# Optimization experiments

Measured on AMD Instinct MI355X. Metric: run time of the kernel, lower is better.

## Reference

```python
import jax, jax.numpy as jnp
import numpy as np

FEATURE_DIM = 128
NUM_EDGES = 640000
NUM_NODES = 40000


def setup_inputs() -> dict:
    key = jax.random.key(0)
    ks = jax.random.split(key, 10)
    d = FEATURE_DIM
    scale = 1.0 / np.sqrt(d)
    inp = {
        "messages": jax.random.normal(ks[0], (NUM_EDGES, d), dtype=jnp.float32),
        "receivers": jax.random.randint(ks[1], (NUM_EDGES,), 0, NUM_NODES, dtype=jnp.int32),
        "num_segments": NUM_NODES,
        "Wk": jax.random.normal(ks[2], (d, d), dtype=jnp.float32) * scale,
        "bk": jnp.zeros((d,), dtype=jnp.float32),
        "Wv": jax.random.normal(ks[3], (d, d), dtype=jnp.float32) * scale,
        "bv": jnp.zeros((d,), dtype=jnp.float32),
        "Wq": jax.random.normal(ks[4], (d, d), dtype=jnp.float32) * scale,
        "bq": jnp.zeros((d,), dtype=jnp.float32),
        "Wo": jax.random.normal(ks[5], (d, d), dtype=jnp.float32) * scale,
        "bo": jnp.zeros((d,), dtype=jnp.float32),
    }
    return inp


def reference(messages, receivers, num_segments, Wk, bk, Wv, bv, Wq, bq, Wo, bo):
    d = messages.shape[-1]
    # per-edge key/value projections
    keys = messages @ Wk + bk            # [E, d]
    values = messages @ Wv + bv          # [E, d]
    # node-level summed messages -> queries
    summed = jax.ops.segment_sum(messages, receivers, num_segments)  # [N, d]
    queries = summed @ Wq + bq                                       # [N, d]
    # scalar attention score per edge (dot over full feature dim)
    msg_q = queries[receivers]                                       # [E, d]
    scores = jnp.sum(msg_q * keys, axis=-1) / jnp.sqrt(jnp.float32(d))  # [E]
    # segment softmax over edges sharing a receiver
    max_s = jax.ops.segment_max(scores, receivers, num_segments)     # [N]
    exp_s = jnp.exp(scores - max_s[receivers])                       # [E]
    sum_e = jax.ops.segment_sum(exp_s, receivers, num_segments)      # [N]
    attn = exp_s / (sum_e[receivers] + 1e-08)                        # [E]
    # weighted scatter-sum of values, then output projection
    agg = jax.ops.segment_sum(values * attn[:, None], receivers, num_segments)  # [N, d]
    return agg @ Wo + bo
```

## Files before the change

### kernel.cpp

```cpp
#include <hip/hip_runtime.h>

#define D 128
#define RSQRT_D 0.088388347648318440550f
#define NEG_HUGE -3.4e38f
#define NPB 8
#define CAP 288
#define DTHR 20.0f

#define FMA4(acc, s, b) { acc.x += (s)*(b).x; acc.y += (s)*(b).y; acc.z += (s)*(b).z; acc.w += (s)*(b).w; }
#define ADD4(acc, b) { acc.x += (b).x; acc.y += (b).y; acc.z += (b).z; acc.w += (b).w; }
#define MRG4(a) { a.x += __shfl_xor(a.x,32); a.y += __shfl_xor(a.y,32); a.z += __shfl_xor(a.z,32); a.w += __shfl_xor(a.w,32); }
#define SCL4(a, f) { a.x *= (f); a.y *= (f); a.z *= (f); a.w *= (f); }
#define Z4 make_float4(0.f,0.f,0.f,0.f)

#define MERGE_HALVES(mi, si, ci) { \
    float mo_ = __shfl_xor(mi, 32); \
    float so_ = __shfl_xor(si, 32); \
    float4 co_; co_.x = __shfl_xor(ci.x, 32); co_.y = __shfl_xor(ci.y, 32); \
    co_.z = __shfl_xor(ci.z, 32); co_.w = __shfl_xor(ci.w, 32); \
    float mt_ = fmaxf(mi, mo_); \
    float e0_ = __expf(mi - mt_), e1_ = __expf(mo_ - mt_); \
    si = si * e0_ + so_ * e1_; \
    ci.x = ci.x * e0_ + co_.x * e1_; ci.y = ci.y * e0_ + co_.y * e1_; \
    ci.z = ci.z * e0_ + co_.z * e1_; ci.w = ci.w * e0_ + co_.w * e1_; \
}

__global__ __launch_bounds__(256) void prep_kernel(
    const float* __restrict__ Wq, const float* __restrict__ Wk,
    const float* __restrict__ bq, const float* __restrict__ bk,
    const float* __restrict__ Wv, const float* __restrict__ Wo,
    const float* __restrict__ bv,
    float* __restrict__ Wqk, float* __restrict__ bqk,
    float* __restrict__ wqb, float* __restrict__ bqb,
    float* __restrict__ Wvo, float* __restrict__ bvo,
    int* __restrict__ zbase, int zcount) {
    int bid = blockIdx.x, t = threadIdx.x;
    if (bid < 64) {
        int i = bid * 2 + (t >> 7), j = t & 127;
        float a1 = 0.f, a2 = 0.f;
        for (int u = 0; u < D; ++u) {
            a1 += Wq[i * D + u] * Wk[j * D + u];
            a2 += Wv[i * D + u] * Wo[u * D + j];
        }
        Wqk[i * D + j] = a1;
        Wvo[i * D + j] = a2;
    } else if (bid == 64) {
        if (t < D) {
            int j = t;
            float a1 = 0.f, a2 = 0.f, a3 = 0.f;
            for (int u = 0; u < D; ++u) {
                a1 += bq[u] * Wk[j * D + u];
                a2 += Wq[j * D + u] * bk[u];
                a3 += bv[u] * Wo[u * D + j];
            }
            bqk[j] = a1; wqb[j] = a2; bvo[j] = a3;
            if (j == 0) {
                float b = 0.f;
                for (int u = 0; u < D; ++u) b += bq[u] * bk[u];
                *bqb = b;
            }
        }
    } else {
        int idx = (bid - 65) * 256 + t;
        if (idx < zcount) zbase[idx] = 0;
    }
}

__global__ void hist_kernel(const int* __restrict__ recv, int* __restrict__ cnt, int E) {
    int i = blockIdx.x * blockDim.x + threadIdx.x;
    int base = i << 2;
    if (base + 3 < E) {
        int4 r = *(const int4*)(recv + base);
        atomicAdd(&cnt[r.x], 1);
        atomicAdd(&cnt[r.y], 1);
        atomicAdd(&cnt[r.z], 1);
        atomicAdd(&cnt[r.w], 1);
    } else {
        for (int u = base; u < E; ++u) atomicAdd(&cnt[recv[u]], 1);
    }
}

__global__ __launch_bounds__(1024) void scan_kernel(const int* __restrict__ cnt,
                                                    int* __restrict__ start, int N) {
    __shared__ int wsum[16];
    __shared__ int chunk_total;
    int t = threadIdx.x;
    int w = t >> 6, lane = t & 63;
    int running = 0;
    const int4* cnt4 = (const int4*)cnt;
    int nIter = (N + 4095) >> 12;
    int4 v = make_int4(0, 0, 0, 0);
    {
        int i = t << 2;
        if (i < N) v = cnt4[i >> 2];
    }
    for (int it = 0; it < nIter; ++it) {
        int4 vn = make_int4(0, 0, 0, 0);
        {
            int i = ((it + 1) << 12) + (t << 2);
            if (it + 1 < nIter && i < N) vn = cnt4[i >> 2];
        }
        int s0 = v.x, s1 = s0 + v.y, s2 = s1 + v.z, s3 = s2 + v.w;
        int x = s3;
#pragma unroll
        for (int off = 1; off < 64; off <<= 1) {
            int y = __shfl_up(x, off);
            if (lane >= off) x += y;
        }
        if (lane == 63) wsum[w] = x;
        __syncthreads();
        if (w == 0 && lane < 16) {
            int s = wsum[lane];
#pragma unroll
            for (int off = 1; off < 16; off <<= 1) {
                int y = __shfl_up(s, off);
                if (lane >= off) s += y;
            }
            wsum[lane] = s;
            if (lane == 15) chunk_total = s;
        }
        __syncthreads();
        int waveoff = (w == 0) ? 0 : wsum[w - 1];
        int tb = running + waveoff + (x - s3);
        int i = (it << 12) + (t << 2);
        if (i < N) ((int4*)start)[i >> 2] = make_int4(tb, tb + s0, tb + s1, tb + s2);
        running += chunk_total;
        __syncthreads();
        v = vn;
    }
    if (t == 0) start[N] = running;
}

__global__ void fill_kernel(const int* __restrict__ recv, const int* __restrict__ start,
                            int* __restrict__ cursor, int* __restrict__ eidx, int E) {
    int e = blockIdx.x * blockDim.x + threadIdx.x;
    if (e >= E) return;
    int r = recv[e];
    int p = atomicAdd(&cursor[r], 1);
    eidx[start[r] + p] = e;
}

__device__ __forceinline__ float hdot32(float4 f, float4 q) {
    float p = f.x * q.x + f.y * q.y + f.z * q.z + f.w * q.w;
    p += __shfl_xor(p, 1); p += __shfl_xor(p, 2); p += __shfl_xor(p, 4);
    p += __shfl_xor(p, 8); p += __shfl_xor(p, 16);
    return p;
}

#define P1STEP(u, Fx) { \
    int r = j + h + 2 * (u); \
    float4 g_ = Fx; \
    float mk_ = (r < b4) ? 1.f : 0.f; \
    g_.x *= mk_; g_.y *= mk_; g_.z *= mk_; g_.w *= mk_; \
    if (r < b1)      { ADD4(a0, g_); } \
    else if (r < b2) { ADD4(a1, g_); } \
    else if (r < b3) { ADD4(a2, g_); } \
    else             { ADD4(a3, g_); } \
}

#define P3STEP(u, Fx) { \
    int r = j + h + 2 * (u); \
    bool valid_ = r < b4; \
    float4 f_ = Fx; \
    float4 qv_ = (r < b1) ? q0 : (r < b2) ? q1 : (r < b3) ? q2 : q3; \
    float qbv_ = (r < b1) ? qb0 : (r < b2) ? qb1 : (r < b3) ? qb2 : qb3; \
    float sc_ = (hdot32(f_, qv_) + qbv_) * RSQRT_D; \
    float msel_ = (r < b1) ? m0 : (r < b2) ? m1 : (r < b3) ? m2 : m3; \
    if (valid_ && sc_ > msel_ + DTHR) { \
        float fac_ = __expf(msel_ - sc_); \
        if (r < b1)      { sm0 *= fac_; SCL4(c0, fac_); m0 = sc_; } \
        else if (r < b2) { sm1 *= fac_; SCL4(c1, fac_); m1 = sc_; } \
        else if (r < b3) { sm2 *= fac_; SCL4(c2, fac_); m2 = sc_; } \
        else             { sm3 *= fac_; SCL4(c3, fac_); m3 = sc_; } \
        msel_ = sc_; \
    } \
    float wgt_ = valid_ ? __expf(sc_ - msel_) : 0.f; \
    if (r < b1)      { sm0 += wgt_; FMA4(c0, wgt_, f_); } \
    else if (r < b2) { sm1 += wgt_; FMA4(c1, wgt_, f_); } \
    else if (r < b3) { sm2 += wgt_; FMA4(c2, wgt_, f_); } \
    else             { sm3 += wgt_; FMA4(c3, wgt_, f_); } \
}

#define P1G(jo, Ra, Rb, Rc, Rd) { int j = b0 + (jo); P1STEP(0, Ra); P1STEP(1, Rb); P1STEP(2, Rc); P1STEP(3, Rd); }
#define P3G(jo, Ra, Rb, Rc, Rd) { int j = b0 + (jo); P3STEP(0, Ra); P3STEP(1, Rb); P3STEP(2, Rc); P3STEP(3, Rd); }

__global__ __launch_bounds__(128, 3) void mega_kernel(
    const float* __restrict__ msg, const int* __restrict__ eidx,
    const int* __restrict__ start,
    const float* __restrict__ Wqk, const float* __restrict__ bqk,
    const float* __restrict__ wqb, const float* __restrict__ bqbp,
    const float* __restrict__ Wvo, const float* __restrict__ bvo,
    const float* __restrict__ bo,
    float* __restrict__ out, int N) {
    __shared__ float4 sums4[NPB * 32];
    __shared__ float4 qks4[NPB * 32];
    __shared__ int eidx_s[CAP];
    __shared__ float sat[NPB];

    int t = threadIdx.x;
    int lane = t & 63, w = t >> 6;
    int h = lane >> 5;
    int k = lane & 31;
    int base = blockIdx.x * NPB;
    const float4* msg4 = (const float4*)msg;

    int nendB = min(base + NPB, N);
    int s0B = start[base];
    int cntB = start[nendB] - s0B;
    int cc = min(cntB, CAP);
    for (int i = t; i < cc; i += 128) eidx_s[i] = eidx[s0B + i];

    int n0 = base + w * 4;
    int b0 = start[min(n0 + 0, N)] - s0B;
    int b1 = start[min(n0 + 1, N)] - s0B;
    int b2 = start[min(n0 + 2, N)] - s0B;
    int b3 = start[min(n0 + 3, N)] - s0B;
    int b4 = start[min(n0 + 4, N)] - s0B;

    __syncthreads();

    auto loadrow = [&](int r) -> float4 {
        int rI = min(r, b4 - 1);
        int e = (rI < CAP) ? eidx_s[rI] : eidx[s0B + rI];
        return msg4[(size_t)e * 32 + k];
    };

    float4 R00 = Z4, R01 = Z4, R02 = Z4, R03 = Z4,
           R10 = Z4, R11 = Z4, R12 = Z4, R13 = Z4,
           R20 = Z4, R21 = Z4, R22 = Z4, R23 = Z4,
           R30 = Z4, R31 = Z4, R32 = Z4, R33 = Z4,
           R40 = Z4, R41 = Z4, R42 = Z4, R43 = Z4,
           R50 = Z4, R51 = Z4, R52 = Z4, R53 = Z4;

    float4 a0 = Z4, a1 = Z4, a2 = Z4, a3 = Z4;
    if (b0 < b4) {
        R00 = loadrow(b0 + h +  0); R01 = loadrow(b0 + h +  2); R02 = loadrow(b0 + h +  4); R03 = loadrow(b0 + h +  6);
        R10 = loadrow(b0 + h +  8); R11 = loadrow(b0 + h + 10); R12 = loadrow(b0 + h + 12); R13 = loadrow(b0 + h + 14);
        R20 = loadrow(b0 + h + 16); R21 = loadrow(b0 + h + 18); R22 = loadrow(b0 + h + 20); R23 = loadrow(b0 + h + 22);
        R30 = loadrow(b0 + h + 24); R31 = loadrow(b0 + h + 26); R32 = loadrow(b0 + h + 28); R33 = loadrow(b0 + h + 30);
        R40 = loadrow(b0 + h + 32); R41 = loadrow(b0 + h + 34); R42 = loadrow(b0 + h + 36); R43 = loadrow(b0 + h + 38);
        R50 = loadrow(b0 + h + 40); R51 = loadrow(b0 + h + 42); R52 = loadrow(b0 + h + 44); R53 = loadrow(b0 + h + 46);
        P1G( 0, R00, R01, R02, R03);
        P1G( 8, R10, R11, R12, R13);
        P1G(16, R20, R21, R22, R23);
        P1G(24, R30, R31, R32, R33);
        P1G(32, R40, R41, R42, R43);
        P1G(40, R50, R51, R52, R53);
        int j = b0 + 48;
        if (j < b4) {
            float4 F0 = loadrow(j + h), F1 = loadrow(j + h + 2);
            for (;;) {
                int jn = j + 4;
                bool more = jn < b4;
                float4 G0, G1;
                if (more) { G0 = loadrow(jn + h); G1 = loadrow(jn + h + 2); }
                P1STEP(0, F0); P1STEP(1, F1);
                if (!more) break;
                F0 = G0; F1 = G1; j = jn;
            }
        }
    }
    MRG4(a0); MRG4(a1); MRG4(a2); MRG4(a3);
    if (lane < 32) {
        sums4[(w * 4 + 0) * 32 + k] = a0;
        sums4[(w * 4 + 1) * 32 + k] = a1;
        sums4[(w * 4 + 2) * 32 + k] = a2;
        sums4[(w * 4 + 3) * 32 + k] = a3;
    }
    __syncthreads();

    {
        int c = t & 31, slot = t >> 5;
        const float4* B4 = (const float4*)Wqk;
        float4 acc0 = ((const float4*)bqk)[c];
        float4 acc1 = acc0;
        for (int i = 0; i < D; i += 4) {
            float4 aA = sums4[slot * 32 + (i >> 2)];
            float4 aB = sums4[(slot + 4) * 32 + (i >> 2)];
            float4 w0 = B4[(i + 0) * 32 + c];
            float4 w1 = B4[(i + 1) * 32 + c];
            float4 w2 = B4[(i + 2) * 32 + c];
            float4 w3 = B4[(i + 3) * 32 + c];
            FMA4(acc0, aA.x, w0); FMA4(acc0, aA.y, w1); FMA4(acc0, aA.z, w2); FMA4(acc0, aA.w, w3);
            FMA4(acc1, aB.x, w0); FMA4(acc1, aB.y, w1); FMA4(acc1, aB.z, w2); FMA4(acc1, aB.w, w3);
        }
        qks4[slot * 32 + c] = acc0;
        qks4[(slot + 4) * 32 + c] = acc1;
    }
    __syncthreads();

    {
        float4 wv = ((const float4*)wqb)[k];
        float bqb = bqbp[0];
        float4 sv0 = sums4[(w * 4 + 0) * 32 + k];
        float4 sv1 = sums4[(w * 4 + 1) * 32 + k];
        float4 sv2 = sums4[(w * 4 + 2) * 32 + k];
        float4 sv3 = sums4[(w * 4 + 3) * 32 + k];
        float qb0 = hdot32(sv0, wv) + bqb;
        float qb1 = hdot32(sv1, wv) + bqb;
        float qb2 = hdot32(sv2, wv) + bqb;
        float qb3 = hdot32(sv3, wv) + bqb;
        float4 q0 = qks4[(w * 4 + 0) * 32 + k];
        float4 q1 = qks4[(w * 4 + 1) * 32 + k];
        float4 q2 = qks4[(w * 4 + 2) * 32 + k];
        float4 q3 = qks4[(w * 4 + 3) * 32 + k];

        float m0 = NEG_HUGE, m1 = NEG_HUGE, m2 = NEG_HUGE, m3 = NEG_HUGE;
        float sm0 = 0.f, sm1 = 0.f, sm2 = 0.f, sm3 = 0.f;
        float4 c0 = Z4, c1 = Z4, c2 = Z4, c3 = Z4;
        if (b0 < b4) {
            P3G( 0, R00, R01, R02, R03);
            P3G( 8, R10, R11, R12, R13);
            P3G(16, R20, R21, R22, R23);
            P3G(24, R30, R31, R32, R33);
            P3G(32, R40, R41, R42, R43);
            P3G(40, R50, R51, R52, R53);
            int j = b0 + 48;
            if (j < b4) {
                float4 F0 = loadrow(j + h), F1 = loadrow(j + h + 2);
                for (;;) {
                    int jn = j + 4;
                    bool more = jn < b4;
                    float4 G0, G1;
                    if (more) { G0 = loadrow(jn + h); G1 = loadrow(jn + h + 2); }
                    P3STEP(0, F0); P3STEP(1, F1);
                    if (!more) break;
                    F0 = G0; F1 = G1; j = jn;
                }
            }
        }
        MERGE_HALVES(m0, sm0, c0);
        MERGE_HALVES(m1, sm1, c1);
        MERGE_HALVES(m2, sm2, c2);
        MERGE_HALVES(m3, sm3, c3);
        float inv0 = 1.f / (sm0 + 1e-8f);
        float inv1 = 1.f / (sm1 + 1e-8f);
        float inv2 = 1.f / (sm2 + 1e-8f);
        float inv3 = 1.f / (sm3 + 1e-8f);
        if (lane < 32) {
            sums4[(w * 4 + 0) * 32 + k] = make_float4(c0.x * inv0, c0.y * inv0, c0.z * inv0, c0.w * inv0);
            sums4[(w * 4 + 1) * 32 + k] = make_float4(c1.x * inv1, c1.y * inv1, c1.z * inv1, c1.w * inv1);
            sums4[(w * 4 + 2) * 32 + k] = make_float4(c2.x * inv2, c2.y * inv2, c2.z * inv2, c2.w * inv2);
            sums4[(w * 4 + 3) * 32 + k] = make_float4(c3.x * inv3, c3.y * inv3, c3.z * inv3, c3.w * inv3);
        }
        if (lane == 0) {
            sat[w * 4 + 0] = sm0 * inv0;
            sat[w * 4 + 1] = sm1 * inv1;
            sat[w * 4 + 2] = sm2 * inv2;
            sat[w * 4 + 3] = sm3 * inv3;
        }
    }
    __syncthreads();

    {
        int c = t & 31, slot = t >> 5;
        const float4* B4 = (const float4*)Wvo;
        float4 bo4 = ((const float4*)bo)[c];
        float4 bv4 = ((const float4*)bvo)[c];
        float sa0 = sat[slot], sa1 = sat[slot + 4];
        float4 acc0 = make_float4(bo4.x + sa0 * bv4.x, bo4.y + sa0 * bv4.y,
                                  bo4.z + sa0 * bv4.z, bo4.w + sa0 * bv4.w);
        float4 acc1 = make_float4(bo4.x + sa1 * bv4.x, bo4.y + sa1 * bv4.y,
                                  bo4.z + sa1 * bv4.z, bo4.w + sa1 * bv4.w);
        for (int i = 0; i < D; i += 4) {
            float4 aA = sums4[slot * 32 + (i >> 2)];
            float4 aB = sums4[(slot + 4) * 32 + (i >> 2)];
            float4 d0 = B4[(i + 0) * 32 + c];
            float4 d1 = B4[(i + 1) * 32 + c];
            float4 d2 = B4[(i + 2) * 32 + c];
            float4 d3 = B4[(i + 3) * 32 + c];
            FMA4(acc0, aA.x, d0); FMA4(acc0, aA.y, d1); FMA4(acc0, aA.z, d2); FMA4(acc0, aA.w, d3);
            FMA4(acc1, aB.x, d0); FMA4(acc1, aB.y, d1); FMA4(acc1, aB.z, d2); FMA4(acc1, aB.w, d3);
        }
        int nA = base + slot, nB = base + slot + 4;
        if (nA < N) ((float4*)(out + (size_t)nA * D))[c] = acc0;
        if (nB < N) ((float4*)(out + (size_t)nB * D))[c] = acc1;
    }
}


extern "C" void kernel_launch(void* const* d_in, const int* in_sizes, int n_in,
                              void* d_out, int out_size, void* d_ws, size_t ws_size,
                              hipStream_t stream) {
    const float* msg = (const float*)d_in[0];
    const int* recv = (const int*)d_in[1];
    const float* Wk = (const float*)d_in[3];
    const float* bk = (const float*)d_in[4];
    const float* Wv = (const float*)d_in[5];
    const float* bv = (const float*)d_in[6];
    const float* Wq = (const float*)d_in[7];
    const float* bq = (const float*)d_in[8];
    const float* Wo = (const float*)d_in[9];
    const float* bo = (const float*)d_in[10];
    float* out = (float*)d_out;

    int E = in_sizes[0] / D;
    int N = out_size / D;

    char* wsb = (char*)d_ws;
    size_t o = 0;
    auto alloc = [&](size_t elems) {
        void* p = wsb + o;
        o += (elems * 4 + 63) & ~(size_t)63;
        return p;
    };

    int* cnt    = (int*)alloc(2 * (size_t)N);
    int* cursor = cnt + N;
    int* start  = (int*)alloc(N + 1);
    int* eidx   = (int*)alloc(E);
    float* Wqk  = (float*)alloc(D * D);
    float* bqk  = (float*)alloc(D);
    float* wqb  = (float*)alloc(D);
    float* bqb  = (float*)alloc(1);
    float* Wvo  = (float*)alloc(D * D);
    float* bvo  = (float*)alloc(D);

    int zcount = 2 * N;
    int zblocks = (zcount + 255) / 256;
    prep_kernel<<<65 + zblocks, 256, 0, stream>>>(Wq, Wk, bq, bk, Wv, Wo, bv,
                                                  Wqk, bqk, wqb, bqb, Wvo, bvo,
                                                  cnt, zcount);
    int E4 = (E + 3) / 4;
    int nbE4 = (E4 + 255) / 256;
    hist_kernel<<<nbE4, 256, 0, stream>>>(recv, cnt, E);
    scan_kernel<<<1, 1024, 0, stream>>>(cnt, start, N);
    int nbE = (E + 255) / 256;
    fill_kernel<<<nbE, 256, 0, stream>>>(recv, start, cursor, eidx, E);
    mega_kernel<<<(N + NPB - 1) / NPB, 128, 0, stream>>>(msg, eidx, start, Wqk, bqk, wqb, bqb,
                                                         Wvo, bvo, bo, out, N);
}
```

Measured before the change: 680.7 us.

## Stream edge rows through an async global-to-LDS ring instead of register caching

Drops the 24 float4 rows each lane kept in registers between the summation pass and the softmax pass. Both passes now stream edge rows through an 8-deep per-wave LDS ring, filled with global_load_lds and throttled by explicit vmcnt waits. The lower register pressure lets the launch bound rise from 3 to 4 blocks per CU. In exchange, the second pass re-reads message rows from memory, relying on L2 hits. There is also a possible race where a ring slot is reused right after it is read, with no explicit LDS wait.

```diff
diff --git a/kernel.cpp b/kernel.cpp
--- a/kernel.cpp
+++ b/kernel.cpp
@@ -12,6 +12,14 @@
 #define MRG4(a) { a.x += __shfl_xor(a.x,32); a.y += __shfl_xor(a.y,32); a.z += __shfl_xor(a.z,32); a.w += __shfl_xor(a.w,32); }
 #define SCL4(a, f) { a.x *= (f); a.y *= (f); a.z *= (f); a.w *= (f); }
 #define Z4 make_float4(0.f,0.f,0.f,0.f)
+
+#define VMCNT7() asm volatile("s_waitcnt vmcnt(7)" ::: "memory")
+#define VMCNT0() asm volatile("s_waitcnt vmcnt(0)" ::: "memory")
+
+__device__ __forceinline__ void gld_lds16(const void* g, void* l) {
+    __builtin_amdgcn_global_load_lds((const __attribute__((address_space(1))) void*)g,
+                                     (__attribute__((address_space(3))) void*)l, 16, 0, 0);
+}
 
 #define MERGE_HALVES(mi, si, ci) { \
     float mo_ = __shfl_xor(mi, 32); \
@@ -147,8 +155,8 @@
     return p;
 }
 
-#define P1STEP(u, Fx) { \
-    int r = j + h + 2 * (u); \
+#define P1ROW(jj, Fx) { \
+    int r = (jj) + h; \
     float4 g_ = Fx; \
     float mk_ = (r < b4) ? 1.f : 0.f; \
     g_.x *= mk_; g_.y *= mk_; g_.z *= mk_; g_.w *= mk_; \
@@ -158,8 +166,8 @@
     else             { ADD4(a3, g_); } \
 }
 
-#define P3STEP(u, Fx) { \
-    int r = j + h + 2 * (u); \
+#define P3ROW(jj, Fx) { \
+    int r = (jj) + h; \
     bool valid_ = r < b4; \
     float4 f_ = Fx; \
     float4 qv_ = (r < b1) ? q0 : (r < b2) ? q1 : (r < b3) ? q2 : q3; \
@@ -181,10 +189,7 @@
     else             { sm3 += wgt_; FMA4(c3, wgt_, f_); } \
 }
 
-#define P1G(jo, Ra, Rb, Rc, Rd) { int j = b0 + (jo); P1STEP(0, Ra); P1STEP(1, Rb); P1STEP(2, Rc); P1STEP(3, Rd); }
-#define P3G(jo, Ra, Rb, Rc, Rd) { int j = b0 + (jo); P3STEP(0, Ra); P3STEP(1, Rb); P3STEP(2, Rc); P3STEP(3, Rd); }
-
-__global__ __launch_bounds__(128, 3) void mega_kernel(
+__global__ __launch_bounds__(128, 4) void mega_kernel(
     const float* __restrict__ msg, const int* __restrict__ eidx,
     const int* __restrict__ start,
     const float* __restrict__ Wqk, const float* __restrict__ bqk,
@@ -192,6 +197,7 @@
     const float* __restrict__ Wvo, const float* __restrict__ bvo,
     const float* __restrict__ bo,
     float* __restrict__ out, int N) {
+    __shared__ float4 ring4[2][8][64];
     __shared__ float4 sums4[NPB * 32];
     __shared__ float4 qks4[NPB * 32];
     __shared__ int eidx_s[CAP];
@@ -207,6 +213,7 @@
     int nendB = min(base + NPB, N);
     int s0B = start[base];
     int cntB = start[nendB] - s0B;
+    bool staged = (cntB <= CAP);
     int cc = min(cntB, CAP);
     for (int i = t; i < cc; i += 128) eidx_s[i] = eidx[s0B + i];
 
@@ -216,48 +223,46 @@
     int b2 = start[min(n0 + 2, N)] - s0B;
     int b3 = start[min(n0 + 3, N)] - s0B;
     int b4 = start[min(n0 + 4, N)] - s0B;
+    int PP = (b4 - b0 + 1) >> 1;
 
     __syncthreads();
 
-    auto loadrow = [&](int r) -> float4 {
+    auto issue_pair = [&](int p) {
+        int r = b0 + 2 * p + h;
+        int rI = min(r, b4 - 1);
+        int e = eidx_s[rI];
+        gld_lds16(msg + (size_t)e * D + (k << 2), (void*)&ring4[w][p & 7][0]);
+    };
+    auto ring_row = [&](int p) -> float4 { return ring4[w][p & 7][h * 32 + k]; };
+    auto loadrow_g = [&](int r) -> float4 {
         int rI = min(r, b4 - 1);
         int e = (rI < CAP) ? eidx_s[rI] : eidx[s0B + rI];
         return msg4[(size_t)e * 32 + k];
     };
 
-    float4 R00 = Z4, R01 = Z4, R02 = Z4, R03 = Z4,
-           R10 = Z4, R11 = Z4, R12 = Z4, R13 = Z4,
-           R20 = Z4, R21 = Z4, R22 = Z4, R23 = Z4,
-           R30 = Z4, R31 = Z4, R32 = Z4, R33 = Z4,
-           R40 = Z4, R41 = Z4, R42 = Z4, R43 = Z4,
-           R50 = Z4, R51 = Z4, R52 = Z4, R53 = Z4;
-
     float4 a0 = Z4, a1 = Z4, a2 = Z4, a3 = Z4;
-    if (b0 < b4) {
-        R00 = loadrow(b0 + h +  0); R01 = loadrow(b0 + h +  2); R02 = loadrow(b0 + h +  4); R03 = loadrow(b0 + h +  6);
-        R10 = loadrow(b0 + h +  8); R11 = loadrow(b0 + h + 10); R12 = loadrow(b0 + h + 12); R13 = loadrow(b0 + h + 14);
-        R20 = loadrow(b0 + h + 16); R21 = loadrow(b0 + h + 18); R22 = loadrow(b0 + h + 20); R23 = loadrow(b0 + h + 22);
-        R30 = loadrow(b0 + h + 24); R31 = loadrow(b0 + h + 26); R32 = loadrow(b0 + h + 28); R33 = loadrow(b0 + h + 30);
-        R40 = loadrow(b0 + h + 32); R41 = loadrow(b0 + h + 34); R42 = loadrow(b0 + h + 36); R43 = loadrow(b0 + h + 38);
-        R50 = loadrow(b0 + h + 40); R51 = loadrow(b0 + h + 42); R52 = loadrow(b0 + h + 44); R53 = loadrow(b0 + h + 46);
-        P1G( 0, R00, R01, R02, R03);
-        P1G( 8, R10, R11, R12, R13);
-        P1G(16, R20, R21, R22, R23);
-        P1G(24, R30, R31, R32, R33);
-        P1G(32, R40, R41, R42, R43);
-        P1G(40, R50, R51, R52, R53);
-        int j = b0 + 48;
-        if (j < b4) {
-            float4 F0 = loadrow(j + h), F1 = loadrow(j + h + 2);
-            for (;;) {
-                int jn = j + 4;
-                bool more = jn < b4;
-                float4 G0, G1;
-                if (more) { G0 = loadrow(jn + h); G1 = loadrow(jn + h + 2); }
-                P1STEP(0, F0); P1STEP(1, F1);
-                if (!more) break;
-                F0 = G0; F1 = G1; j = jn;
-            }
+    if (staged) {
+        if (PP > 0) {
+            int pre = min(PP, 8);
+            for (int p = 0; p < pre; ++p) issue_pair(p);
+            int pmain = PP - 8;
+            int p = 0;
+            for (; p < pmain; ++p) {
+                VMCNT7();
+                float4 f = ring_row(p);
+                P1ROW(b0 + 2 * p, f);
+                issue_pair(p + 8);
+            }
+            VMCNT0();
+            for (; p < PP; ++p) {
+                float4 f = ring_row(p);
+                P1ROW(b0 + 2 * p, f);
+            }
+        }
+    } else {
+        for (int r0 = b0; r0 < b4; r0 += 2) {
+            float4 g = loadrow_g(r0 + h);
+            P1ROW(r0, g);
         }
     }
     MRG4(a0); MRG4(a1); MRG4(a2); MRG4(a3);
@@ -290,6 +295,10 @@
     __syncthreads();
 
     {
+        if (staged && PP > 0) {
+            int pre = min(PP, 8);
+            for (int p = 0; p < pre; ++p) issue_pair(p);
+        }
         float4 wv = ((const float4*)wqb)[k];
         float bqb = bqbp[0];
         float4 sv0 = sums4[(w * 4 + 0) * 32 + k];
@@ -308,25 +317,26 @@
         float m0 = NEG_HUGE, m1 = NEG_HUGE, m2 = NEG_HUGE, m3 = NEG_HUGE;
         float sm0 = 0.f, sm1 = 0.f, sm2 = 0.f, sm3 = 0.f;
         float4 c0 = Z4, c1 = Z4, c2 = Z4, c3 = Z4;
-        if (b0 < b4) {
-            P3G( 0, R00, R01, R02, R03);
-            P3G( 8, R10, R11, R12, R13);
-            P3G(16, R20, R21, R22, R23);
-            P3G(24, R30, R31, R32, R33);
-            P3G(32, R40, R41, R42, R43);
-            P3G(40, R50, R51, R52, R53);
-            int j = b0 + 48;
-            if (j < b4) {
-                float4 F0 = loadrow(j + h), F1 = loadrow(j + h + 2);
-                for (;;) {
-                    int jn = j + 4;
-                    bool more = jn < b4;
-                    float4 G0, G1;
-                    if (more) { G0 = loadrow(jn + h); G1 = loadrow(jn + h + 2); }
-                    P3STEP(0, F0); P3STEP(1, F1);
-                    if (!more) break;
-                    F0 = G0; F1 = G1; j = jn;
+        if (staged) {
+            if (PP > 0) {
+                int pmain = PP - 8;
+                int p = 0;
+                for (; p < pmain; ++p) {
+                    VMCNT7();
+                    float4 f = ring_row(p);
+                    P3ROW(b0 + 2 * p, f);
+                    issue_pair(p + 8);
                 }
+                VMCNT0();
+                for (; p < PP; ++p) {
+                    float4 f = ring_row(p);
+                    P3ROW(b0 + 2 * p, f);
+                }
+            }
+        } else {
+            for (int r0 = b0; r0 < b4; r0 += 2) {
+                float4 g = loadrow_g(r0 + h);
+                P3ROW(r0, g);
             }
         }
         MERGE_HALVES(m0, sm0, c0);
```

Result: slower. 697.3 us (+2.4%).
